# Kernel optimization log

Hardware: AMD Instinct MI355X
Metric: run time of the kernel (lower is better)

## Reference

```python
import jax, jax.numpy as jnp
import numpy as np

W = 4  # kernel_size

def setup_inputs() -> dict:
    key = jax.random.key(0)
    k1, k2, k3, k4 = jax.random.split(key, 4)
    B, T, D, H = 4, 4096, 2048, 256
    x = jax.random.normal(k1, (B, T, D), dtype=jnp.float32)
    # stored as [in, out] (transpose of torch Linear convention)
    w1 = jax.random.normal(k2, (D, H), dtype=jnp.float32) * 0.02
    w2 = jax.random.normal(k3, (H, D * W), dtype=jnp.float32) * 0.02
    b2 = jax.random.normal(k4, (D * W,), dtype=jnp.float32) * 0.02
    return {"x": x, "w1": w1, "w2": w2, "b2": b2}

def reference(x, w1, w2, b2):
    # x: [B, T, D]
    B, T, D = x.shape
    # kernel generator: Linear -> silu -> Linear(+bias)
    h = jax.nn.silu(jnp.einsum('btd,dh->bth', x, w1))
    flat = jnp.einsum('bth,ho->bto', h, w2) + b2          # [B, T, D*W]
    kernels = flat.reshape(B, T, D, W)                    # per-token depthwise kernels
    # causal depthwise dynamic conv: out[t] = sum_w k[t, :, w] * x[t - (W-1) + w]
    xp = jnp.pad(x, ((0, 0), (W - 1, 0), (0, 0)))         # left-pad time by W-1
    out = jnp.zeros_like(x)
    for w in range(W):  # W is a small static constant (4)
        out = out + kernels[..., w] * xp[:, w:w + T, :]
    return jax.nn.silu(out)
```

## Files before the change

kernel.cpp:

```cpp
#include <hip/hip_runtime.h>

typedef unsigned short u16;
typedef unsigned int   u32;
typedef __attribute__((ext_vector_type(8))) short short8;
typedef __attribute__((ext_vector_type(4))) float floatx4;

#define T_DIM 4096
#define D_DIM 2048
#define H_DIM 256
#define M_DIM 16384
#define NFLAT 8192

__device__ __forceinline__ u16 f2bf(float f) {
  union { float f; u32 u; } c; c.f = f;
  u32 x = c.u;
  x += 0x7FFFu + ((x >> 16) & 1u);
  return (u16)(x >> 16);
}
__device__ __forceinline__ u32 pk2(float a, float b) {
  return (u32)f2bf(a) | ((u32)f2bf(b) << 16);
}

__device__ __forceinline__ void glds16(const void* g, void* l) {
  __builtin_amdgcn_global_load_lds(
      (const __attribute__((address_space(1))) void*)g,
      (__attribute__((address_space(3))) void*)l, 16, 0, 0);
}

__global__ void __launch_bounds__(256) tr_cvt_all(const float* __restrict__ w1,
                                                  u16* __restrict__ w1t,
                                                  const float* __restrict__ w2,
                                                  u16* __restrict__ w2t) {
  __shared__ u16 tile[32][33];
  int bid = blockIdx.x;
  const float* src; u16* dst; int R, C, c0, r0;
  if (bid < 512) {
    src = w1; dst = w1t; R = D_DIM; C = H_DIM;
    c0 = (bid & 7) * 32; r0 = (bid >> 3) * 32;
  } else {
    int b = bid - 512;
    src = w2; dst = w2t; R = H_DIM; C = NFLAT;
    c0 = (b & 255) * 32; r0 = (b >> 8) * 32;
  }
  const int tx = threadIdx.x & 31;
  const int ty = threadIdx.x >> 5;
  #pragma unroll
  for (int i = ty; i < 32; i += 8)
    tile[i][tx] = f2bf(src[(size_t)(r0 + i) * C + (c0 + tx)]);
  __syncthreads();
  #pragma unroll
  for (int i = ty; i < 32; i += 8)
    dst[(size_t)(c0 + i) * R + (r0 + tx)] = tile[tx][i];
}

__global__ void __launch_bounds__(256) gemm1_silu(const float* __restrict__ X,
                                                  const u16* __restrict__ Bt,
                                                  u16* __restrict__ H) {
  __shared__ __align__(16) u16 As[2][64][64];
  __shared__ __align__(16) u16 Bs[2][128][64];
  const int tid  = threadIdx.x;
  const int lane = tid & 63, l15 = lane & 15, quad = lane >> 4;
  const int wv   = tid >> 6, wy = wv >> 1, wx = wv & 1;
  const int m0   = blockIdx.y * 64;
  const int n0   = blockIdx.x * 128;
  const int srow = lane >> 3, sc = lane & 7;

  floatx4 acc[2][4];
  const floatx4 zf = {0.f, 0.f, 0.f, 0.f};
  #pragma unroll
  for (int i = 0; i < 2; ++i)
    #pragma unroll
    for (int j = 0; j < 4; ++j) acc[i][j] = zf;

  float4 fA[2][2];

#define G1_LOADA(KT)                                                          \
  _Pragma("unroll")                                                           \
  for (int i = 0; i < 2; ++i) {                                               \
    int s = i * 256 + tid, row = s >> 3, g = s & 7;                           \
    const float* xs = &X[(size_t)(m0 + row) * D_DIM + (KT) * 64 + g * 8];     \
    fA[i][0] = *(const float4*)xs;                                            \
    fA[i][1] = *(const float4*)(xs + 4);                                      \
  }

#define G1_WRITEA(BUF)                                                        \
  _Pragma("unroll")                                                           \
  for (int i = 0; i < 2; ++i) {                                               \
    int s = i * 256 + tid, row = s >> 3, g = s & 7, c = g ^ (row & 7);        \
    uint4 pk;                                                                 \
    pk.x = pk2(fA[i][0].x, fA[i][0].y);                                       \
    pk.y = pk2(fA[i][0].z, fA[i][0].w);                                       \
    pk.z = pk2(fA[i][1].x, fA[i][1].y);                                       \
    pk.w = pk2(fA[i][1].z, fA[i][1].w);                                       \
    *(uint4*)&As[BUF][row][c * 8] = pk;                                       \
  }

#define G1_STAGEB(KT, BUF)                                                    \
  _Pragma("unroll")                                                           \
  for (int ci = 0; ci < 4; ++ci) {                                            \
    int ch  = ci * 4 + wv;                                                    \
    int row = ch * 8 + srow;                                                  \
    glds16(&Bt[(size_t)(n0 + row) * D_DIM + (KT) * 64 + (sc ^ (row & 7)) * 8],\
           (char*)Bs + (BUF) * 16384 + ch * 1024);                            \
  }

  G1_LOADA(0);
  G1_STAGEB(0, 0);
  G1_WRITEA(0);
  G1_LOADA(1);
  __syncthreads();

  #pragma unroll 2
  for (int t = 0; t < 32; ++t) {
    const int b = t & 1;
    if (t + 1 < 32) {
      G1_WRITEA(b ^ 1);
      G1_STAGEB(t + 1, b ^ 1);
    }
    if (t + 2 < 32) G1_LOADA(t + 2);
    short8 af[2][2], bfr[4][2];
    #pragma unroll
    for (int ks = 0; ks < 2; ++ks) {
      #pragma unroll
      for (int mi = 0; mi < 2; ++mi) {
        int row = wy * 32 + mi * 16 + l15;
        af[mi][ks] = *(const short8*)&As[b][row][((ks * 4 + quad) ^ (row & 7)) * 8];
      }
      #pragma unroll
      for (int ni = 0; ni < 4; ++ni) {
        int row = wx * 64 + ni * 16 + l15;
        bfr[ni][ks] = *(const short8*)&Bs[b][row][((ks * 4 + quad) ^ (row & 7)) * 8];
      }
    }
    #pragma unroll
    for (int ks = 0; ks < 2; ++ks)
      #pragma unroll
      for (int mi = 0; mi < 2; ++mi)
        #pragma unroll
        for (int ni = 0; ni < 4; ++ni)
          acc[mi][ni] = __builtin_amdgcn_mfma_f32_16x16x32_bf16(af[mi][ks], bfr[ni][ks], acc[mi][ni], 0, 0, 0);
    if (t + 1 < 32) __syncthreads();
  }

  #pragma unroll
  for (int mi = 0; mi < 2; ++mi)
    #pragma unroll
    for (int ni = 0; ni < 4; ++ni)
      #pragma unroll
      for (int r = 0; r < 4; ++r) {
        float v = acc[mi][ni][r];
        v = v / (1.f + __expf(-v));
        int row = m0 + wy * 32 + mi * 16 + quad * 4 + r;
        int col = n0 + wx * 64 + ni * 16 + l15;
        H[(size_t)row * H_DIM + col] = f2bf(v);
      }
#undef G1_LOADA
#undef G1_WRITEA
#undef G1_STAGEB
}

__global__ void __launch_bounds__(256) gemm2_conv_silu(const u16* __restrict__ Hin,
                                                       const u16* __restrict__ Bt,
                                                       const float* __restrict__ bias,
                                                       const float* __restrict__ X,
                                                       float* __restrict__ Out) {
  __shared__ __align__(16) u16 As[2][128][64];
  __shared__ __align__(16) u16 Bs[2][128][64];
  const int tid  = threadIdx.x;
  const int lane = tid & 63, l15 = lane & 15, quad = lane >> 4;
  const int wv   = tid >> 6, wy = wv >> 1, wx = wv & 1;
  const int m0   = blockIdx.y * 128;
  const int d0   = blockIdx.x * 32;
  const int srow = lane >> 3, sc = lane & 7;

  floatx4 acc[4][4];
  const floatx4 zf = {0.f, 0.f, 0.f, 0.f};
  #pragma unroll
  for (int i = 0; i < 4; ++i)
    #pragma unroll
    for (int j = 0; j < 4; ++j) acc[i][j] = zf;

#define G2_STAGE(KT, BUF)                                                     \
  _Pragma("unroll")                                                           \
  for (int ci = 0; ci < 4; ++ci) {                                            \
    int ch  = ci * 4 + wv;                                                    \
    int row = ch * 8 + srow;                                                  \
    int g   = (sc ^ (row & 7)) * 8;                                           \
    glds16(&Hin[(size_t)(m0 + row) * H_DIM + (KT) * 64 + g],                  \
           (char*)As + (BUF) * 16384 + ch * 1024);                            \
    int fc = (d0 + ((row >> 6) << 4) + (row & 15)) * 4 + ((row >> 4) & 3);    \
    glds16(&Bt[(size_t)fc * H_DIM + (KT) * 64 + g],                           \
           (char*)Bs + (BUF) * 16384 + ch * 1024);                            \
  }

  G2_STAGE(0, 0);
  __syncthreads();

  #pragma unroll
  for (int t = 0; t < 4; ++t) {
    const int b = t & 1;
    if (t + 1 < 4) G2_STAGE(t + 1, b ^ 1);
    short8 af[4][2], bfr[4][2];
    #pragma unroll
    for (int ks = 0; ks < 2; ++ks) {
      #pragma unroll
      for (int mi = 0; mi < 4; ++mi) {
        int row = wy * 64 + mi * 16 + l15;
        af[mi][ks] = *(const short8*)&As[b][row][((ks * 4 + quad) ^ (row & 7)) * 8];
      }
      #pragma unroll
      for (int ni = 0; ni < 4; ++ni) {
        int row = wx * 64 + ni * 16 + l15;
        bfr[ni][ks] = *(const short8*)&Bs[b][row][((ks * 4 + quad) ^ (row & 7)) * 8];
      }
    }
    #pragma unroll
    for (int ks = 0; ks < 2; ++ks)
      #pragma unroll
      for (int mi = 0; mi < 4; ++mi)
        #pragma unroll
        for (int ni = 0; ni < 4; ++ni)
          acc[mi][ni] = __builtin_amdgcn_mfma_f32_16x16x32_bf16(af[mi][ks], bfr[ni][ks], acc[mi][ni], 0, 0, 0);
    if (t + 1 < 4) __syncthreads();
  }
#undef G2_STAGE

  const int d     = d0 + wx * 16 + l15;
  const float4 bv = *(const float4*)&bias[(size_t)d * 4];
  const int tbase = m0 & (T_DIM - 1);
  const int bbase = m0 - tbase;
  const float* xcol = &X[(size_t)bbase * D_DIM + d];
  float* ocol       = &Out[(size_t)m0 * D_DIM + d];

  #pragma unroll
  for (int mi = 0; mi < 4; ++mi) {
    int t0 = wy * 64 + mi * 16 + quad * 4;
    int tq = tbase + t0;
    float xv[7];
    #pragma unroll
    for (int j = 0; j < 7; ++j) {
      int tt = tq - 3 + j;
      xv[j] = (tt >= 0) ? xcol[(size_t)tt * D_DIM] : 0.f;
    }
    #pragma unroll
    for (int r = 0; r < 4; ++r) {
      float c0 = acc[mi][0][r] + bv.x;
      float c1 = acc[mi][1][r] + bv.y;
      float c2 = acc[mi][2][r] + bv.z;
      float c3 = acc[mi][3][r] + bv.w;
      float o  = c0 * xv[r] + c1 * xv[r + 1] + c2 * xv[r + 2] + c3 * xv[r + 3];
      float y  = o / (1.f + __expf(-o));
      ocol[(size_t)(t0 + r) * D_DIM] = y;
    }
  }
}

extern "C" void kernel_launch(void* const* d_in, const int* in_sizes, int n_in,
                              void* d_out, int out_size, void* d_ws, size_t ws_size,
                              hipStream_t stream) {
  const float* x  = (const float*)d_in[0];
  const float* w1 = (const float*)d_in[1];
  const float* w2 = (const float*)d_in[2];
  const float* b2 = (const float*)d_in[3];
  float* out = (float*)d_out;

  u16* w1t = (u16*)d_ws;
  u16* w2t = w1t + (size_t)H_DIM * D_DIM;
  u16* h   = w2t + (size_t)NFLAT * H_DIM;

  tr_cvt_all<<<512 + 2048, 256, 0, stream>>>(w1, w1t, w2, w2t);
  gemm1_silu<<<dim3(2, M_DIM / 64), 256, 0, stream>>>(x, w1t, h);
  gemm2_conv_silu<<<dim3(D_DIM / 32, M_DIM / 128), 256, 0, stream>>>(h, w2t, b2, x, out);
}
```

Baseline: 369.0 us.

## Shrink gemm1 N-tile, remap workgroups by XCD, single-buffer gemm2 LDS

gemm1 now uses a 64x64 output tile instead of 64x128 and launches twice as many workgroups. The aim is more parallelism and less LDS per block. Both GEMMs remap the linear block index so that consecutive blocks, assumed to be dealt round-robin across the 8 XCDs, share M rows for L2 locality. gemm2 drops double buffering for a simple single-buffer loop with two barriers per K step, which frees LDS for occupancy but removes load/compute overlap. A side effect is that each X row in gemm1 is now read and converted four times rather than twice.

```diff
diff --git a/kernel.cpp b/kernel.cpp
--- a/kernel.cpp
+++ b/kernel.cpp
@@ -57,20 +57,22 @@
                                                   const u16* __restrict__ Bt,
                                                   u16* __restrict__ H) {
   __shared__ __align__(16) u16 As[2][64][64];
-  __shared__ __align__(16) u16 Bs[2][128][64];
+  __shared__ __align__(16) u16 Bs[2][64][64];
   const int tid  = threadIdx.x;
   const int lane = tid & 63, l15 = lane & 15, quad = lane >> 4;
   const int wv   = tid >> 6, wy = wv >> 1, wx = wv & 1;
-  const int m0   = blockIdx.y * 64;
-  const int n0   = blockIdx.x * 128;
+  const int lin  = blockIdx.x + blockIdx.y * 4;
+  const int wgid = (lin & 7) * 128 + (lin >> 3);
+  const int m0   = (wgid >> 2) * 64;
+  const int n0   = (wgid & 3) * 64;
   const int srow = lane >> 3, sc = lane & 7;
 
-  floatx4 acc[2][4];
+  floatx4 acc[2][2];
   const floatx4 zf = {0.f, 0.f, 0.f, 0.f};
   #pragma unroll
   for (int i = 0; i < 2; ++i)
     #pragma unroll
-    for (int j = 0; j < 4; ++j) acc[i][j] = zf;
+    for (int j = 0; j < 2; ++j) acc[i][j] = zf;
 
   float4 fA[2][2];
 
@@ -97,11 +99,11 @@
 
 #define G1_STAGEB(KT, BUF)                                                    \
   _Pragma("unroll")                                                           \
-  for (int ci = 0; ci < 4; ++ci) {                                            \
-    int ch  = ci * 4 + wv;                                                    \
+  for (int ci = 0; ci < 2; ++ci) {                  \
+    int ch  = wv * 2 + ci;                                                    \
     int row = ch * 8 + srow;                                                  \
     glds16(&Bt[(size_t)(n0 + row) * D_DIM + (KT) * 64 + (sc ^ (row & 7)) * 8],\
-           (char*)Bs + (BUF) * 16384 + ch * 1024);                            \
+           (char*)Bs + (BUF) * 8192 + ch * 1024);                             \
   }
 
   G1_LOADA(0);
@@ -118,7 +120,7 @@
       G1_STAGEB(t + 1, b ^ 1);
     }
     if (t + 2 < 32) G1_LOADA(t + 2);
-    short8 af[2][2], bfr[4][2];
+    short8 af[2][2], bfr[2][2];
     #pragma unroll
     for (int ks = 0; ks < 2; ++ks) {
       #pragma unroll
@@ -127,8 +129,8 @@
         af[mi][ks] = *(const short8*)&As[b][row][((ks * 4 + quad) ^ (row & 7)) * 8];
       }
       #pragma unroll
-      for (int ni = 0; ni < 4; ++ni) {
-        int row = wx * 64 + ni * 16 + l15;
+      for (int ni = 0; ni < 2; ++ni) {
+        int row = wx * 32 + ni * 16 + l15;
         bfr[ni][ks] = *(const short8*)&Bs[b][row][((ks * 4 + quad) ^ (row & 7)) * 8];
       }
     }
@@ -137,7 +139,7 @@
       #pragma unroll
       for (int mi = 0; mi < 2; ++mi)
         #pragma unroll
-        for (int ni = 0; ni < 4; ++ni)
+        for (int ni = 0; ni < 2; ++ni)
           acc[mi][ni] = __builtin_amdgcn_mfma_f32_16x16x32_bf16(af[mi][ks], bfr[ni][ks], acc[mi][ni], 0, 0, 0);
     if (t + 1 < 32) __syncthreads();
   }
@@ -145,13 +147,13 @@
   #pragma unroll
   for (int mi = 0; mi < 2; ++mi)
     #pragma unroll
-    for (int ni = 0; ni < 4; ++ni)
+    for (int ni = 0; ni < 2; ++ni)
       #pragma unroll
       for (int r = 0; r < 4; ++r) {
         float v = acc[mi][ni][r];
         v = v / (1.f + __expf(-v));
         int row = m0 + wy * 32 + mi * 16 + quad * 4 + r;
-        int col = n0 + wx * 64 + ni * 16 + l15;
+        int col = n0 + wx * 32 + ni * 16 + l15;
         H[(size_t)row * H_DIM + col] = f2bf(v);
       }
 #undef G1_LOADA
@@ -164,13 +166,15 @@
                                                        const float* __restrict__ bias,
                                                        const float* __restrict__ X,
                                                        float* __restrict__ Out) {
-  __shared__ __align__(16) u16 As[2][128][64];
-  __shared__ __align__(16) u16 Bs[2][128][64];
+  __shared__ __align__(16) u16 As[128][64];
+  __shared__ __align__(16) u16 Bs[128][64];
   const int tid  = threadIdx.x;
   const int lane = tid & 63, l15 = lane & 15, quad = lane >> 4;
   const int wv   = tid >> 6, wy = wv >> 1, wx = wv & 1;
-  const int m0   = blockIdx.y * 128;
-  const int d0   = blockIdx.x * 32;
+  const int lin  = blockIdx.x + blockIdx.y * 64;
+  const int wgid = (lin & 7) * 1024 + (lin >> 3);
+  const int m0   = (wgid >> 6) * 128;
+  const int d0   = (wgid & 63) * 32;
   const int srow = lane >> 3, sc = lane & 7;
 
   floatx4 acc[4][4];
@@ -180,38 +184,30 @@
     #pragma unroll
     for (int j = 0; j < 4; ++j) acc[i][j] = zf;
 
-#define G2_STAGE(KT, BUF)                                                     \
-  _Pragma("unroll")                                                           \
-  for (int ci = 0; ci < 4; ++ci) {                                            \
-    int ch  = ci * 4 + wv;                                                    \
-    int row = ch * 8 + srow;                                                  \
-    int g   = (sc ^ (row & 7)) * 8;                                           \
-    glds16(&Hin[(size_t)(m0 + row) * H_DIM + (KT) * 64 + g],                  \
-           (char*)As + (BUF) * 16384 + ch * 1024);                            \
-    int fc = (d0 + ((row >> 6) << 4) + (row & 15)) * 4 + ((row >> 4) & 3);    \
-    glds16(&Bt[(size_t)fc * H_DIM + (KT) * 64 + g],                           \
-           (char*)Bs + (BUF) * 16384 + ch * 1024);                            \
-  }
-
-  G2_STAGE(0, 0);
-  __syncthreads();
-
-  #pragma unroll
-  for (int t = 0; t < 4; ++t) {
-    const int b = t & 1;
-    if (t + 1 < 4) G2_STAGE(t + 1, b ^ 1);
+  for (int k0 = 0; k0 < H_DIM; k0 += 64) {
+    __syncthreads();
+    #pragma unroll
+    for (int ci = 0; ci < 4; ++ci) {
+      int ch  = ci * 4 + wv;
+      int row = ch * 8 + srow;
+      int g   = (sc ^ (row & 7)) * 8;
+      glds16(&Hin[(size_t)(m0 + row) * H_DIM + k0 + g], (char*)As + ch * 1024);
+      int fc = (d0 + ((row >> 6) << 4) + (row & 15)) * 4 + ((row >> 4) & 3);
+      glds16(&Bt[(size_t)fc * H_DIM + k0 + g], (char*)Bs + ch * 1024);
+    }
+    __syncthreads();
     short8 af[4][2], bfr[4][2];
     #pragma unroll
     for (int ks = 0; ks < 2; ++ks) {
       #pragma unroll
       for (int mi = 0; mi < 4; ++mi) {
         int row = wy * 64 + mi * 16 + l15;
-        af[mi][ks] = *(const short8*)&As[b][row][((ks * 4 + quad) ^ (row & 7)) * 8];
+        af[mi][ks] = *(const short8*)&As[row][((ks * 4 + quad) ^ (row & 7)) * 8];
       }
       #pragma unroll
       for (int ni = 0; ni < 4; ++ni) {
         int row = wx * 64 + ni * 16 + l15;
-        bfr[ni][ks] = *(const short8*)&Bs[b][row][((ks * 4 + quad) ^ (row & 7)) * 8];
+        bfr[ni][ks] = *(const short8*)&Bs[row][((ks * 4 + quad) ^ (row & 7)) * 8];
       }
     }
     #pragma unroll
@@ -221,9 +217,7 @@
         #pragma unroll
         for (int ni = 0; ni < 4; ++ni)
           acc[mi][ni] = __builtin_amdgcn_mfma_f32_16x16x32_bf16(af[mi][ks], bfr[ni][ks], acc[mi][ni], 0, 0, 0);
-    if (t + 1 < 4) __syncthreads();
-  }
-#undef G2_STAGE
+  }
 
   const int d     = d0 + wx * 16 + l15;
   const float4 bv = *(const float4*)&bias[(size_t)d * 4];
@@ -269,6 +263,6 @@
   u16* h   = w2t + (size_t)NFLAT * H_DIM;
 
   tr_cvt_all<<<512 + 2048, 256, 0, stream>>>(w1, w1t, w2, w2t);
-  gemm1_silu<<<dim3(2, M_DIM / 64), 256, 0, stream>>>(x, w1t, h);
+  gemm1_silu<<<dim3(4, M_DIM / 64), 256, 0, stream>>>(x, w1t, h);
   gemm2_conv_silu<<<dim3(D_DIM / 32, M_DIM / 128), 256, 0, stream>>>(h, w2t, b2, x, out);
 }
```

After: 380.8 us. 1.03x slower.
